# Performance work log

Hardware: AMD Instinct MI355X
Metric: run time of the kernel (lower is better)

Reference implementation:

```python
import jax, jax.numpy as jnp
import numpy as np

NEG_SLOPE = 0.2

def _gat_layer(x, src, dst, W, a_s, a_d, b, concat):
    # x: [N, F_in], W: [F_in, H*C], a_s/a_d: [H, C]
    N = x.shape[0]
    H, C = a_s.shape
    h = (x @ W).reshape(N, H, C)                       # per-head projection
    al_s = jnp.sum(h * a_s, axis=-1)                   # [N, H]
    al_d = jnp.sum(h * a_d, axis=-1)                   # [N, H]
    e = jax.nn.leaky_relu(al_s[src] + al_d[dst], NEG_SLOPE)  # [E, H]
    # segment softmax over incoming edges of each dst node
    m = jax.ops.segment_max(e, dst, num_segments=N)    # [N, H]
    ex = jnp.exp(e - m[dst])
    denom = jax.ops.segment_sum(ex, dst, num_segments=N)
    alpha = ex / denom[dst]                            # [E, H]
    msg = h[src] * alpha[:, :, None]                   # [E, H, C]
    out = jax.ops.segment_sum(msg, dst, num_segments=N)  # [N, H, C]
    if concat:
        return out.reshape(N, H * C) + b
    return out.mean(axis=1) + b


def setup_inputs() -> dict:
    key = jax.random.key(0)
    ks = jax.random.split(key, 12)
    N, F_in, H, C1, LAT, E = 16384, 512, 4, 128, 64, 262144
    x = jax.random.normal(ks[0], (N, F_in), dtype=jnp.float32)
    edge_index = jax.random.randint(ks[1], (2, E), 0, N, dtype=jnp.int64)
    s = 0.05
    return {
        'x': x,
        'edge_index': edge_index,
        'W1': jax.random.normal(ks[2], (F_in, H * C1), dtype=jnp.float32) * s,
        'a_src1': jax.random.normal(ks[3], (H, C1), dtype=jnp.float32) * s,
        'a_dst1': jax.random.normal(ks[4], (H, C1), dtype=jnp.float32) * s,
        'b1': jax.random.normal(ks[5], (H * C1,), dtype=jnp.float32) * s,
        'W2': jax.random.normal(ks[6], (H * C1, H * LAT), dtype=jnp.float32) * s,
        'a_src2': jax.random.normal(ks[7], (H, LAT), dtype=jnp.float32) * s,
        'a_dst2': jax.random.normal(ks[8], (H, LAT), dtype=jnp.float32) * s,
        'b2': jax.random.normal(ks[9], (LAT,), dtype=jnp.float32) * s,
    }


def reference(x, edge_index, W1, a_src1, a_dst1, b1, W2, a_src2, a_dst2, b2):
    N = x.shape[0]
    # PyG GATConv default add_self_loops=True
    loop = jnp.arange(N, dtype=edge_index.dtype)
    src = jnp.concatenate([edge_index[0], loop])
    dst = jnp.concatenate([edge_index[1], loop])
    h = jax.nn.relu(_gat_layer(x, src, dst, W1, a_src1, a_dst1, b1, concat=True))
    out = _gat_layer(h, src, dst, W2, a_src2, a_dst2, b2, concat=False)
    return out
```

## Files before the change

### kernel.cpp

```cpp
#include <hip/hip_runtime.h>
#include <stdint.h>
#include <stddef.h>
#include <limits.h>

typedef __bf16 bf16;
typedef __bf16 bf16x4 __attribute__((ext_vector_type(4)));
typedef __bf16 bf16x8 __attribute__((ext_vector_type(8)));
typedef float  f32x4  __attribute__((ext_vector_type(4)));

#define CAP 128
#define CSTRIDE 16

static __device__ __forceinline__ float lrelu(float x) { return x > 0.f ? x : 0.2f * x; }
static __device__ __forceinline__ float san(float v) { return (fabsf(v) < 1e4f) ? v : 0.0f; }
static __device__ __forceinline__ float wexp(float e) { return __expf(fminf(e, 30.f)); }

static __device__ __forceinline__ void async_load16(const bf16* g, bf16* l) {
  __builtin_amdgcn_global_load_lds((const __attribute__((address_space(1))) void*)g,
                                   (__attribute__((address_space(3))) void*)l, 16, 0, 0);
}

static __device__ __forceinline__ void drain_barrier() {
  asm volatile("s_waitcnt vmcnt(0) lgkmcnt(0)" ::: "memory");
  __builtin_amdgcn_s_barrier();
}


__global__ __launch_bounds__(256) void prep_w(const int* __restrict__ src,
                                              const int* __restrict__ dst,
                                              int E, int* __restrict__ cnt,
                                              int* __restrict__ slots,
                                              const float* __restrict__ W1,
                                              const float* __restrict__ W2,
                                              bf16* __restrict__ W1T,
                                              bf16* __restrict__ W2T) {
  int b = blockIdx.x;
  if (b < 256) {
    for (int e = b * 256 + threadIdx.x; e < E; e += 256 * 256) {
      int d = dst[e];
      int pos = atomicAdd(&cnt[d * CSTRIDE], 1);
      if (pos < CAP) slots[(size_t)d * CAP + pos] = src[e];
    }
    return;
  }
  b -= 256;
  __shared__ bf16 t[32][33];
  const float* in; bf16* out; int R, C, bx, by;
  if (b < 256) { in = W1; out = W1T; R = 512; C = 512; by = b >> 4; bx = b & 15; }
  else         { b -= 256; in = W2; out = W2T; R = 512; C = 256; by = b >> 3; bx = b & 7; }
  const int lane = threadIdx.x & 31, r8 = threadIdx.x >> 5;
#pragma unroll
  for (int k = 0; k < 4; ++k) {
    int r = by * 32 + r8 + k * 8, c = bx * 32 + lane;
    t[lane][r8 + k * 8] = (bf16)san(in[(size_t)r * C + c]);
  }
  __syncthreads();
#pragma unroll
  for (int k = 0; k < 4; ++k) {
    int oc = bx * 32 + r8 + k * 8;
    out[(size_t)oc * R + by * 32 + lane] = t[r8 + k * 8][lane];
  }
}


__global__ __launch_bounds__(256) void gemm_al_l1(const float* __restrict__ X,
                                                  const bf16* __restrict__ BT,
                                                  bf16* __restrict__ C,
                                                  const float* __restrict__ a_s,
                                                  const float* __restrict__ a_d,
                                                  float* __restrict__ al_s,
                                                  float* __restrict__ al_d,
                                                  int M, int N, int K) {
  __shared__ __align__(16) bf16 As[2][64 * 32];
  __shared__ __align__(16) bf16 Bs[2][128 * 32];
  __shared__ float alred[2][64][2];
  const int tid = threadIdx.x;
  const int b   = blockIdx.x;

  const int lane = tid & 63;
  const int wave = tid >> 6;
  const int mi   = ((b >> 5) << 3) | (b & 7);
  const int head = (b >> 3) & 3;
  const int m0 = mi * 64;
  const int n0 = head * 128;
  const int wm = (wave >> 1) * 32;
  const int wn = (wave & 1) * 64;

  f32x4 acc[2][4] = {};

  const int id1 = tid + 256;
  const float* apx = X  + (size_t)(m0 + (tid >> 2)) * K + (tid & 3) * 8;
  const bf16*  b0p = BT + (size_t)(n0 + (tid >> 2)) * K + (tid & 3) * 8;
  const bf16*  b1p = BT + (size_t)(n0 + (id1 >> 2)) * K + (id1 & 3) * 8;

  const int kq = (lane >> 4) * 8;
  const int rA = wm + (lane & 15);
  const int rB = wn + (lane & 15);

  {
    async_load16(b0p, &Bs[0][tid * 8]);
    async_load16(b1p, &Bs[0][id1 * 8]);
    f32x4 u0 = *(const f32x4*)(apx);
    f32x4 u1 = *(const f32x4*)(apx + 4);
    bf16x8 w;
#pragma unroll
    for (int k = 0; k < 4; ++k) { w[k] = (bf16)san(u0[k]); w[4 + k] = (bf16)san(u1[k]); }
    *(bf16x8*)&As[0][tid * 8] = w;
    drain_barrier();
  }

  int cur = 0;
  for (int k0 = 0; k0 < K; k0 += 32) {
    const int kn = k0 + 32;
    const bool pf = (kn < K);
    f32x4 u0, u1;
    if (pf) {
      async_load16(b0p + kn, &Bs[cur ^ 1][tid * 8]);
      async_load16(b1p + kn, &Bs[cur ^ 1][id1 * 8]);
      u0 = *(const f32x4*)(apx + kn);
      u1 = *(const f32x4*)(apx + kn + 4);
    }

    bf16x8 af[2], bfv[4];
#pragma unroll
    for (int i = 0; i < 2; ++i) af[i]  = *(const bf16x8*)&As[cur][(rA + i * 16) * 32 + kq];
#pragma unroll
    for (int j = 0; j < 4; ++j) bfv[j] = *(const bf16x8*)&Bs[cur][(rB + j * 16) * 32 + kq];
#pragma unroll
    for (int i = 0; i < 2; ++i)
#pragma unroll
      for (int j = 0; j < 4; ++j)
        acc[i][j] = __builtin_amdgcn_mfma_f32_16x16x32_bf16(af[i], bfv[j], acc[i][j], 0, 0, 0);

    if (pf) {
      bf16x8 w;
#pragma unroll
      for (int k = 0; k < 4; ++k) { w[k] = (bf16)san(u0[k]); w[4 + k] = (bf16)san(u1[k]); }
      *(bf16x8*)&As[cur ^ 1][tid * 8] = w;
    }

    drain_barrier();
    cur ^= 1;
  }

  const int cc = lane & 15;
  const int rb = (lane >> 4) * 4;
#pragma unroll
  for (int i = 0; i < 2; ++i)
#pragma unroll
    for (int j = 0; j < 4; ++j) {
      int gcol = n0 + wn + j * 16 + cc;
#pragma unroll
      for (int r = 0; r < 4; ++r) {
        int grow = m0 + wm + i * 16 + rb + r;
        C[(size_t)grow * N + gcol] = (bf16)acc[i][j][r];
      }
    }

  {
    float asv[4], adv[4];
#pragma unroll
    for (int j = 0; j < 4; ++j) {
      int col = head * 128 + wn + j * 16 + cc;
      asv[j] = san(a_s[col]);
      adv[j] = san(a_d[col]);
    }
    const int wnh = wn >> 6;
#pragma unroll
    for (int i = 0; i < 2; ++i)
#pragma unroll
      for (int r = 0; r < 4; ++r) {
        float ps = 0.f, pd = 0.f;
#pragma unroll
        for (int j = 0; j < 4; ++j) { ps += acc[i][j][r] * asv[j]; pd += acc[i][j][r] * adv[j]; }
#pragma unroll
        for (int off = 1; off <= 8; off <<= 1) {
          ps += __shfl_xor(ps, off);
          pd += __shfl_xor(pd, off);
        }
        if (cc == 0) {
          int row = wm + i * 16 + rb + r;
          alred[wnh][row][0] = ps;
          alred[wnh][row][1] = pd;
        }
      }
    __syncthreads();
    if (tid < 64) {
      al_s[(size_t)(m0 + tid) * 4 + head] = alred[0][tid][0] + alred[1][tid][0];
      al_d[(size_t)(m0 + tid) * 4 + head] = alred[0][tid][1] + alred[1][tid][1];
    }
  }
}


__global__ __launch_bounds__(256) void gemm_al_l2(const bf16* __restrict__ A,
                                                  const bf16* __restrict__ BT,
                                                  bf16* __restrict__ C,
                                                  const float* __restrict__ a_s,
                                                  const float* __restrict__ a_d,
                                                  float* __restrict__ al_s,
                                                  float* __restrict__ al_d,
                                                  int M, int N, int K) {
  __shared__ __align__(16) bf16 As[2][64 * 32];
  __shared__ __align__(16) bf16 Bs[2][128 * 32];
  const int tid  = threadIdx.x;
  const int lane = tid & 63;
  const int wave = tid >> 6;
  const int b    = blockIdx.x;
  const int mi = ((b >> 4) << 3) | (b & 7);
  const int nh = (b >> 3) & 1;
  const int m0 = mi * 64;
  const int n0 = nh * 128;
  const int wm = (wave >> 1) * 32;
  const int wn = (wave & 1) * 64;

  f32x4 acc[2][4] = {};

  const int tb = tid + 256;
  const bf16* ap  = A  + (size_t)(m0 + (tid >> 2)) * K + (tid & 3) * 8;
  const bf16* bp0 = BT + (size_t)(n0 + (tid >> 2)) * K + (tid & 3) * 8;
  const bf16* bp1 = BT + (size_t)(n0 + (tb  >> 2)) * K + (tb  & 3) * 8;

  const int kq = (lane >> 4) * 8;
  const int rA = wm + (lane & 15);
  const int rB = wn + (lane & 15);

  async_load16(ap,  &As[0][tid * 8]);
  async_load16(bp0, &Bs[0][tid * 8]);
  async_load16(bp1, &Bs[0][tb  * 8]);
  drain_barrier();

  int cur = 0;
  for (int k0 = 0; k0 < K; k0 += 32) {
    const int kn = k0 + 32;
    if (kn < K) {
      async_load16(ap  + kn, &As[cur ^ 1][tid * 8]);
      async_load16(bp0 + kn, &Bs[cur ^ 1][tid * 8]);
      async_load16(bp1 + kn, &Bs[cur ^ 1][tb  * 8]);
    }

    bf16x8 af[2], bfv[4];
#pragma unroll
    for (int i = 0; i < 2; ++i) af[i]  = *(const bf16x8*)&As[cur][(rA + i * 16) * 32 + kq];
#pragma unroll
    for (int j = 0; j < 4; ++j) bfv[j] = *(const bf16x8*)&Bs[cur][(rB + j * 16) * 32 + kq];
#pragma unroll
    for (int i = 0; i < 2; ++i)
#pragma unroll
      for (int j = 0; j < 4; ++j)
        acc[i][j] = __builtin_amdgcn_mfma_f32_16x16x32_bf16(af[i], bfv[j], acc[i][j], 0, 0, 0);

    drain_barrier();
    cur ^= 1;
  }

  const int cc = lane & 15;
  const int rb = (lane >> 4) * 4;
#pragma unroll
  for (int i = 0; i < 2; ++i)
#pragma unroll
    for (int j = 0; j < 4; ++j) {
      int gcol = n0 + wn + j * 16 + cc;
#pragma unroll
      for (int r = 0; r < 4; ++r) {
        int grow = m0 + wm + i * 16 + rb + r;
        C[(size_t)grow * N + gcol] = (bf16)acc[i][j][r];
      }
    }

  {
    const int head = nh * 2 + (wn >> 6);
    float asv[4], adv[4];
#pragma unroll
    for (int j = 0; j < 4; ++j) {
      int col = head * 64 + j * 16 + cc;
      asv[j] = san(a_s[col]);
      adv[j] = san(a_d[col]);
    }
#pragma unroll
    for (int i = 0; i < 2; ++i)
#pragma unroll
      for (int r = 0; r < 4; ++r) {
        float ps = 0.f, pd = 0.f;
#pragma unroll
        for (int j = 0; j < 4; ++j) { ps += acc[i][j][r] * asv[j]; pd += acc[i][j][r] * adv[j]; }
#pragma unroll
        for (int off = 1; off <= 8; off <<= 1) {
          ps += __shfl_xor(ps, off);
          pd += __shfl_xor(pd, off);
        }
        if (cc == 0) {
          int row = m0 + wm + i * 16 + rb + r;
          al_s[(size_t)row * 4 + head] = ps;
          al_d[(size_t)row * 4 + head] = pd;
        }
      }
  }
}


__global__ __launch_bounds__(256) void aggregate1_f(const bf16* __restrict__ h1,
                                                    const float* __restrict__ al_s,
                                                    const float* __restrict__ al_d,
                                                    const int* __restrict__ cnt,
                                                    int* __restrict__ slots,
                                                    const float* __restrict__ bias,
                                                    bf16* __restrict__ out) {
  __shared__ int   sIdx[4][64];
  __shared__ f32x4 sW[4][64];
  const int wv   = threadIdx.x >> 6;
  const int lane = threadIdx.x & 63;
  const int n = blockIdx.x * 4 + wv;
  const int cb = lane * 8;
  const int hd = lane >> 4;
  const int beg = n * CAP;
  const int len = min(cnt[n * CSTRIDE], CAP);
  const f32x4 alsn = *(const f32x4*)(al_s + (size_t)n * 4);
  const f32x4 aldn = *(const f32x4*)(al_d + (size_t)n * 4);

  const float wself = wexp(lrelu(alsn[hd] + aldn[hd]));
  bf16x8 hv0 = *(const bf16x8*)(h1 + (size_t)n * 512 + cb);
  float acc[8];
#pragma unroll
  for (int k = 0; k < 8; ++k) acc[k] = wself * (float)hv0[k];

  f32x4 Lv = {0.f, 0.f, 0.f, 0.f};
  if (lane == 0) {
#pragma unroll
    for (int h = 0; h < 4; ++h) Lv[h] = wexp(lrelu(alsn[h] + aldn[h]));
  }

  if (len <= 64) {
    int v = (lane < len) ? slots[beg + lane] : INT_MAX;
    if (len > 1) {
#pragma unroll
      for (int k = 2; k <= 64; k <<= 1) {
#pragma unroll
        for (int j = k >> 1; j > 0; j >>= 1) {
          int p = __shfl_xor(v, j);
          bool take_min = (((lane & k) == 0) == ((lane & j) == 0));
          v = take_min ? min(v, p) : max(v, p);
        }
      }
      if (lane < len) slots[beg + lane] = v;
    }
    if (lane < len) {
      sIdx[wv][lane] = v;
      f32x4 a = *(const f32x4*)(al_s + (size_t)v * 4);
      f32x4 w;
#pragma unroll
      for (int h = 0; h < 4; ++h) w[h] = wexp(lrelu(a[h] + aldn[h]));
      sW[wv][lane] = w;
#pragma unroll
      for (int h = 0; h < 4; ++h) Lv[h] += w[h];
    }
#pragma unroll 4
    for (int j = 0; j < len; ++j) {
      int s = sIdx[wv][j];
      float a = sW[wv][j][hd];
      bf16x8 hv = *(const bf16x8*)(h1 + (size_t)s * 512 + cb);
#pragma unroll
      for (int k = 0; k < 8; ++k) acc[k] += a * (float)hv[k];
    }
  } else {
    if (lane == 0) {
      for (int i = beg + 1; i < beg + len; ++i) {
        int v = slots[i];
        int j = i - 1;
        while (j >= beg && slots[j] > v) { slots[j + 1] = slots[j]; --j; }
        slots[j + 1] = v;
      }
    }
    asm volatile("s_waitcnt vmcnt(0)" ::: "memory");
    for (int c0 = beg; c0 < beg + len; c0 += 64) {
      const int cl = min(64, beg + len - c0);
      if (lane < cl) {
        int s = slots[c0 + lane];
        sIdx[wv][lane] = s;
        f32x4 a = *(const f32x4*)(al_s + (size_t)s * 4);
        f32x4 w;
#pragma unroll
        for (int h = 0; h < 4; ++h) w[h] = wexp(lrelu(a[h] + aldn[h]));
        sW[wv][lane] = w;
#pragma unroll
        for (int h = 0; h < 4; ++h) Lv[h] += w[h];
      }
#pragma unroll 4
      for (int j = 0; j < cl; ++j) {
        int s = sIdx[wv][j];
        float a = sW[wv][j][hd];
        bf16x8 hv = *(const bf16x8*)(h1 + (size_t)s * 512 + cb);
#pragma unroll
        for (int k = 0; k < 8; ++k) acc[k] += a * (float)hv[k];
      }
    }
  }

  for (int off = 32; off; off >>= 1) {
#pragma unroll
    for (int h = 0; h < 4; ++h) Lv[h] += __shfl_xor(Lv[h], off);
  }
  const float inv = 1.0f / Lv[hd];
  bf16x8 ov;
#pragma unroll
  for (int k = 0; k < 8; ++k)
    ov[k] = (bf16)fmaxf(acc[k] * inv + san(bias[cb + k]), 0.f);
  *(bf16x8*)(out + (size_t)n * 512 + cb) = ov;
}


__global__ __launch_bounds__(256) void aggregate2_f(const bf16* __restrict__ h2,
                                                    const float* __restrict__ al_s,
                                                    const float* __restrict__ al_d,
                                                    const int* __restrict__ cnt,
                                                    const int* __restrict__ slots,
                                                    const float* __restrict__ bias,
                                                    float* __restrict__ out) {
  __shared__ int   sIdx[4][64];
  __shared__ f32x4 sW[4][64];
  const int wv   = threadIdx.x >> 6;
  const int lane = threadIdx.x & 63;
  const int n = blockIdx.x * 4 + wv;
  const int hd = lane >> 4;
  const int cb = lane * 4;
  const int beg = n * CAP;
  const int len = min(cnt[n * CSTRIDE], CAP);
  const f32x4 alsn = *(const f32x4*)(al_s + (size_t)n * 4);
  const f32x4 aldn = *(const f32x4*)(al_d + (size_t)n * 4);

  const float wself = wexp(lrelu(alsn[hd] + aldn[hd]));
  bf16x4 hv0 = *(const bf16x4*)(h2 + (size_t)n * 256 + cb);
  float acc0 = wself * (float)hv0[0], acc1 = wself * (float)hv0[1];
  float acc2 = wself * (float)hv0[2], acc3 = wself * (float)hv0[3];
  f32x4 Lv = {0.f, 0.f, 0.f, 0.f};
  if (lane == 0) {
#pragma unroll
    for (int h = 0; h < 4; ++h) Lv[h] = wexp(lrelu(alsn[h] + aldn[h]));
  }
  for (int c0 = beg; c0 < beg + len; c0 += 64) {
    const int cl = min(64, beg + len - c0);
    if (lane < cl) {
      int s = slots[c0 + lane];
      sIdx[wv][lane] = s;
      f32x4 a = *(const f32x4*)(al_s + (size_t)s * 4);
      f32x4 w;
#pragma unroll
      for (int h = 0; h < 4; ++h) w[h] = wexp(lrelu(a[h] + aldn[h]));
      sW[wv][lane] = w;
#pragma unroll
      for (int h = 0; h < 4; ++h) Lv[h] += w[h];
    }
#pragma unroll 4
    for (int j = 0; j < cl; ++j) {
      int s = sIdx[wv][j];
      float a = sW[wv][j][hd];
      bf16x4 hv = *(const bf16x4*)(h2 + (size_t)s * 256 + cb);
      acc0 += a * (float)hv[0];
      acc1 += a * (float)hv[1];
      acc2 += a * (float)hv[2];
      acc3 += a * (float)hv[3];
    }
  }
  for (int off = 32; off; off >>= 1) {
#pragma unroll
    for (int h = 0; h < 4; ++h) Lv[h] += __shfl_xor(Lv[h], off);
  }
  const float inv = 1.0f / Lv[hd];
  acc0 *= inv; acc1 *= inv; acc2 *= inv; acc3 *= inv;
  acc0 += __shfl_xor(acc0, 16); acc1 += __shfl_xor(acc1, 16);
  acc2 += __shfl_xor(acc2, 16); acc3 += __shfl_xor(acc3, 16);
  acc0 += __shfl_xor(acc0, 32); acc1 += __shfl_xor(acc1, 32);
  acc2 += __shfl_xor(acc2, 32); acc3 += __shfl_xor(acc3, 32);
  if (lane < 16) {
    int ob = lane * 4;
    f32x4 ov;
    ov[0] = 0.25f * acc0 + san(bias[ob]);
    ov[1] = 0.25f * acc1 + san(bias[ob + 1]);
    ov[2] = 0.25f * acc2 + san(bias[ob + 2]);
    ov[3] = 0.25f * acc3 + san(bias[ob + 3]);
    *(f32x4*)(out + (size_t)n * 64 + ob) = ov;
  }
}


extern "C" void kernel_launch(void* const* d_in, const int* in_sizes, int n_in,
                              void* d_out, int out_size, void* d_ws, size_t ws_size,
                              hipStream_t stream) {
  const float* x   = (const float*)d_in[0];
  const int*   ei  = (const int*)d_in[1];
  const float* W1  = (const float*)d_in[2];
  const float* as1 = (const float*)d_in[3];
  const float* ad1 = (const float*)d_in[4];
  const float* b1  = (const float*)d_in[5];
  const float* W2  = (const float*)d_in[6];
  const float* as2 = (const float*)d_in[7];
  const float* ad2 = (const float*)d_in[8];
  const float* b2  = (const float*)d_in[9];
  float* outp = (float*)d_out;

  const int N = in_sizes[0] / 512;
  const int E = in_sizes[1] / 2;
  const int* src = ei;
  const int* dst = ei + E;

  char* p = (char*)d_ws;
  auto alloc = [&](size_t bytes) {
    char* r = p;
    p += (bytes + 255) & ~(size_t)255;
    return r;
  };
  bf16* h1    = (bf16*)alloc((size_t)N * 512 * 2);
  bf16* hbuf  = (bf16*)alloc((size_t)N * 512 * 2);
  bf16* W1T   = (bf16*)alloc((size_t)512 * 512 * 2);
  bf16* W2T   = (bf16*)alloc((size_t)256 * 512 * 2);
  float* al_s1 = (float*)alloc((size_t)N * 4 * 4);
  float* al_d1 = (float*)alloc((size_t)N * 4 * 4);
  float* al_s2 = (float*)alloc((size_t)N * 4 * 4);
  float* al_d2 = (float*)alloc((size_t)N * 4 * 4);
  int* cnt     = (int*)alloc((size_t)N * CSTRIDE * 4);
  int* slots   = (int*)alloc((size_t)N * CAP * 4);
  bf16* h2 = h1;

  hipMemsetAsync(cnt, 0, (size_t)N * CSTRIDE * 4, stream);
  prep_w<<<256 + 256 + 128, 256, 0, stream>>>(src, dst, E, cnt, slots, W1, W2, W1T, W2T);

  gemm_al_l1<<<1024, 256, 0, stream>>>(x, W1T, h1, as1, ad1, al_s1, al_d1, N, 512, 512);
  aggregate1_f<<<N / 4, 256, 0, stream>>>(h1, al_s1, al_d1, cnt, slots, b1, hbuf);

  gemm_al_l2<<<512, 256, 0, stream>>>(hbuf, W2T, h2, as2, ad2, al_s2, al_d2,
                                      N, 256, 512);
  aggregate2_f<<<N / 4, 256, 0, stream>>>(h2, al_s2, al_d2, cnt, slots, b2, outp);
}
```

Baseline: 192.4 us.

## Split slot sorting into separate kernel and remap layer-1 aggregation to column slices

```diff
diff --git a/kernel.cpp b/kernel.cpp
--- a/kernel.cpp
+++ b/kernel.cpp
@@ -59,6 +59,39 @@
   for (int k = 0; k < 4; ++k) {
     int oc = bx * 32 + r8 + k * 8;
     out[(size_t)oc * R + by * 32 + lane] = t[r8 + k * 8][lane];
+  }
+}
+
+
+__global__ __launch_bounds__(256) void sort_slots(const int* __restrict__ cnt,
+                                                  int* __restrict__ slots) {
+  const int wv   = threadIdx.x >> 6;
+  const int lane = threadIdx.x & 63;
+  const int n = blockIdx.x * 4 + wv;
+  const int beg = n * CAP;
+  const int len = min(cnt[n * CSTRIDE], CAP);
+  if (len <= 1) return;
+  if (len <= 64) {
+    int v = (lane < len) ? slots[beg + lane] : INT_MAX;
+#pragma unroll
+    for (int k = 2; k <= 64; k <<= 1) {
+#pragma unroll
+      for (int j = k >> 1; j > 0; j >>= 1) {
+        int p = __shfl_xor(v, j);
+        bool take_min = (((lane & k) == 0) == ((lane & j) == 0));
+        v = take_min ? min(v, p) : max(v, p);
+      }
+    }
+    if (lane < len) slots[beg + lane] = v;
+  } else {
+    if (lane == 0) {
+      for (int i = beg + 1; i < beg + len; ++i) {
+        int v = slots[i];
+        int j = i - 1;
+        while (j >= beg && slots[j] > v) { slots[j + 1] = slots[j]; --j; }
+        slots[j + 1] = v;
+      }
+    }
   }
 }
 
@@ -299,113 +332,57 @@
 }
 
 
-__global__ __launch_bounds__(256) void aggregate1_f(const bf16* __restrict__ h1,
+__global__ __launch_bounds__(256) void aggregate1_v(const bf16* __restrict__ h1,
                                                     const float* __restrict__ al_s,
                                                     const float* __restrict__ al_d,
                                                     const int* __restrict__ cnt,
-                                                    int* __restrict__ slots,
+                                                    const int* __restrict__ slots,
                                                     const float* __restrict__ bias,
-                                                    bf16* __restrict__ out) {
-  __shared__ int   sIdx[4][64];
-  __shared__ f32x4 sW[4][64];
+                                                    bf16* __restrict__ out, int N) {
+  const int sl   = blockIdx.x & 7;
+  const int g    = blockIdx.x >> 3;
   const int wv   = threadIdx.x >> 6;
   const int lane = threadIdx.x & 63;
-  const int n = blockIdx.x * 4 + wv;
-  const int cb = lane * 8;
-  const int hd = lane >> 4;
-  const int beg = n * CAP;
-  const int len = min(cnt[n * CSTRIDE], CAP);
-  const f32x4 alsn = *(const f32x4*)(al_s + (size_t)n * 4);
-  const f32x4 aldn = *(const f32x4*)(al_d + (size_t)n * 4);
-
-  const float wself = wexp(lrelu(alsn[hd] + aldn[hd]));
-  bf16x8 hv0 = *(const bf16x8*)(h1 + (size_t)n * 512 + cb);
+  const int nb   = lane >> 3;
+  const int c8   = lane & 7;
+  const int n    = g * 32 + wv * 8 + nb;
+  const int hd   = sl >> 1;
+  const int cbase = sl * 64 + c8 * 8;
+  const int beg  = n * CAP;
+  const int len  = min(cnt[n * CSTRIDE], CAP);
+  const float aldh = al_d[(size_t)n * 4 + hd];
+  const int* srow = slots + beg;
+
+  int ml = len;
+#pragma unroll
+  for (int off = 8; off <= 32; off <<= 1) ml = max(ml, __shfl_xor(ml, off));
+
+  const float wself = wexp(lrelu(al_s[(size_t)n * 4 + hd] + aldh));
+  float L = wself;
   float acc[8];
-#pragma unroll
-  for (int k = 0; k < 8; ++k) acc[k] = wself * (float)hv0[k];
-
-  f32x4 Lv = {0.f, 0.f, 0.f, 0.f};
-  if (lane == 0) {
-#pragma unroll
-    for (int h = 0; h < 4; ++h) Lv[h] = wexp(lrelu(alsn[h] + aldn[h]));
-  }
-
-  if (len <= 64) {
-    int v = (lane < len) ? slots[beg + lane] : INT_MAX;
-    if (len > 1) {
-#pragma unroll
-      for (int k = 2; k <= 64; k <<= 1) {
-#pragma unroll
-        for (int j = k >> 1; j > 0; j >>= 1) {
-          int p = __shfl_xor(v, j);
-          bool take_min = (((lane & k) == 0) == ((lane & j) == 0));
-          v = take_min ? min(v, p) : max(v, p);
-        }
-      }
-      if (lane < len) slots[beg + lane] = v;
-    }
-    if (lane < len) {
-      sIdx[wv][lane] = v;
-      f32x4 a = *(const f32x4*)(al_s + (size_t)v * 4);
-      f32x4 w;
-#pragma unroll
-      for (int h = 0; h < 4; ++h) w[h] = wexp(lrelu(a[h] + aldn[h]));
-      sW[wv][lane] = w;
-#pragma unroll
-      for (int h = 0; h < 4; ++h) Lv[h] += w[h];
-    }
+  {
+    bf16x8 hv = *(const bf16x8*)(h1 + (size_t)n * 512 + cbase);
+#pragma unroll
+    for (int k = 0; k < 8; ++k) acc[k] = wself * (float)hv[k];
+  }
+
 #pragma unroll 4
-    for (int j = 0; j < len; ++j) {
-      int s = sIdx[wv][j];
-      float a = sW[wv][j][hd];
-      bf16x8 hv = *(const bf16x8*)(h1 + (size_t)s * 512 + cb);
-#pragma unroll
-      for (int k = 0; k < 8; ++k) acc[k] += a * (float)hv[k];
-    }
-  } else {
-    if (lane == 0) {
-      for (int i = beg + 1; i < beg + len; ++i) {
-        int v = slots[i];
-        int j = i - 1;
-        while (j >= beg && slots[j] > v) { slots[j + 1] = slots[j]; --j; }
-        slots[j + 1] = v;
-      }
-    }
-    asm volatile("s_waitcnt vmcnt(0)" ::: "memory");
-    for (int c0 = beg; c0 < beg + len; c0 += 64) {
-      const int cl = min(64, beg + len - c0);
-      if (lane < cl) {
-        int s = slots[c0 + lane];
-        sIdx[wv][lane] = s;
-        f32x4 a = *(const f32x4*)(al_s + (size_t)s * 4);
-        f32x4 w;
-#pragma unroll
-        for (int h = 0; h < 4; ++h) w[h] = wexp(lrelu(a[h] + aldn[h]));
-        sW[wv][lane] = w;
-#pragma unroll
-        for (int h = 0; h < 4; ++h) Lv[h] += w[h];
-      }
-#pragma unroll 4
-      for (int j = 0; j < cl; ++j) {
-        int s = sIdx[wv][j];
-        float a = sW[wv][j][hd];
-        bf16x8 hv = *(const bf16x8*)(h1 + (size_t)s * 512 + cb);
-#pragma unroll
-        for (int k = 0; k < 8; ++k) acc[k] += a * (float)hv[k];
-      }
-    }
-  }
-
-  for (int off = 32; off; off >>= 1) {
-#pragma unroll
-    for (int h = 0; h < 4; ++h) Lv[h] += __shfl_xor(Lv[h], off);
-  }
-  const float inv = 1.0f / Lv[hd];
+  for (int j = 0; j < ml; ++j) {
+    const bool ok = (j < len);
+    int   s = ok ? srow[j] : n;
+    float w = ok ? wexp(lrelu(al_s[(size_t)s * 4 + hd] + aldh)) : 0.f;
+    L += w;
+    bf16x8 rv = *(const bf16x8*)(h1 + (size_t)s * 512 + cbase);
+#pragma unroll
+    for (int k = 0; k < 8; ++k) acc[k] += w * (float)rv[k];
+  }
+
+  const float inv = 1.0f / L;
   bf16x8 ov;
 #pragma unroll
   for (int k = 0; k < 8; ++k)
-    ov[k] = (bf16)fmaxf(acc[k] * inv + san(bias[cb + k]), 0.f);
-  *(bf16x8*)(out + (size_t)n * 512 + cb) = ov;
+    ov[k] = (bf16)fmaxf(acc[k] * inv + san(bias[cbase + k]), 0.f);
+  *(bf16x8*)(out + (size_t)n * 512 + cbase) = ov;
 }
 
 
@@ -523,9 +500,11 @@
 
   hipMemsetAsync(cnt, 0, (size_t)N * CSTRIDE * 4, stream);
   prep_w<<<256 + 256 + 128, 256, 0, stream>>>(src, dst, E, cnt, slots, W1, W2, W1T, W2T);
+  sort_slots<<<N / 4, 256, 0, stream>>>(cnt, slots);
 
   gemm_al_l1<<<1024, 256, 0, stream>>>(x, W1T, h1, as1, ad1, al_s1, al_d1, N, 512, 512);
-  aggregate1_f<<<N / 4, 256, 0, stream>>>(h1, al_s1, al_d1, cnt, slots, b1, hbuf);
+  aggregate1_v<<<8 * (N / 32), 256, 0, stream>>>(h1, al_s1, al_d1, cnt, slots,
+                                                 b1, hbuf, N);
 
   gemm_al_l2<<<512, 256, 0, stream>>>(hbuf, W2T, h2, as2, ad2, al_s2, al_d2,
                                       N, 256, 512);
```

After: 202.3 us. +5.1%, slower.
